# Optimization experiments

Hardware: AMD Instinct MI355X
Metric: run time of the kernel (lower is better)

The kernel has to match this reference:

```python
import jax, jax.numpy as jnp
import numpy as np

EPS_LN = 1e-5


def fwht(x):
    """Fast Walsh-Hadamard transform over the last axis (power-of-two length).
    Vectorized butterfly: log2(n) stages, each a reshape + add/sub."""
    orig_shape = x.shape
    n = orig_shape[-1]
    y = x.reshape(-1, n)
    h = 1
    while h < n:
        y = y.reshape(-1, n // (2 * h), 2, h)
        a = y[:, :, 0, :]
        b = y[:, :, 1, :]
        y = jnp.stack([a + b, a - b], axis=2).reshape(-1, n)
        h <<= 1
    return y.reshape(orig_shape)


def setup_inputs() -> dict:
    key = jax.random.key(0)
    kx, kw, kg = jax.random.split(key, 3)
    B, S, D_IN, D_OUT = 4, 4096, 2048, 2048
    x = jax.random.normal(kx, (B, S, D_IN), dtype=jnp.float32)
    # kaiming_uniform_(a=sqrt(5)) -> bound = 1/sqrt(in_features)
    bound = 1.0 / np.sqrt(D_IN)
    W = jax.random.uniform(kw, (D_OUT, D_IN), dtype=jnp.float32,
                           minval=-bound, maxval=bound)
    gamma = jnp.ones((D_IN,), dtype=jnp.float32)
    beta = jnp.zeros((D_IN,), dtype=jnp.float32)
    return {"x": x, "W": W, "gamma": gamma, "beta": beta}


def reference(x, W, gamma, beta):
    bits = 4
    max_val = (1 << (bits - 1)) - 1  # 7
    # LayerNorm over last dim
    mu = jnp.mean(x, axis=-1, keepdims=True)
    var = jnp.mean(jnp.square(x - mu), axis=-1, keepdims=True)
    x_ln = (x - mu) * jax.lax.rsqrt(var + EPS_LN) * gamma + beta
    # Activation fake-quant to `bits` bits (per-row absmax scale)
    x_scale = jnp.clip(jnp.max(jnp.abs(x_ln), axis=-1, keepdims=True), 1e-6, None)
    x_int = jnp.clip(jnp.round(x_ln * max_val / x_scale), -max_val, max_val)
    x_q = x_int * x_scale / max_val
    # Hadamard transform of quantized activations
    x_h = fwht(x_q)
    # Ternary weight quantization with global mean-abs scale
    w_scale = jnp.clip(jnp.mean(jnp.abs(W)), 1e-6, None)
    w_q = (jnp.where(W > 0.5 * w_scale, 1.0, 0.0)
           + jnp.where(W < -0.5 * w_scale, -1.0, 0.0)) * w_scale
    # Linear (no bias), then second Hadamard transform
    out = jnp.einsum('bsd,od->bso', x_h, w_q)
    return fwht(out)
```

## Files before the change

### kernel.cpp

```cpp
#include <hip/hip_runtime.h>

typedef unsigned short u16;
typedef __attribute__((ext_vector_type(8))) __bf16 bf16x8;
typedef __attribute__((ext_vector_type(16))) float floatx16;

#define DDIM 2048
#define MROWS 16384
#define BK 64

__device__ __forceinline__ u16 f2bf(float f) {
    unsigned int u = __builtin_bit_cast(unsigned int, f);
    u = (u + 0x7fffu + ((u >> 16) & 1u)) >> 16;
    return (u16)u;
}

__device__ __forceinline__ float wave_sum(float v) {
#pragma unroll
    for (int o = 32; o > 0; o >>= 1) v += __shfl_down(v, o, 64);
    return v;
}
__device__ __forceinline__ float wave_max(float v) {
#pragma unroll
    for (int o = 32; o > 0; o >>= 1) v = fmaxf(v, __shfl_down(v, o, 64));
    return v;
}

__global__ __launch_bounds__(256) void absmean_part(const float4* __restrict__ W4,
                                                    float* __restrict__ partial) {
    float s = 0.f;
    for (int i = blockIdx.x * 256 + threadIdx.x; i < (DDIM * DDIM / 4); i += 1024 * 256) {
        float4 v = W4[i];
        s += fabsf(v.x) + fabsf(v.y) + fabsf(v.z) + fabsf(v.w);
    }
    s = wave_sum(s);
    __shared__ float red[4];
    if ((threadIdx.x & 63) == 0) red[threadIdx.x >> 6] = s;
    __syncthreads();
    if (threadIdx.x == 0) partial[blockIdx.x] = red[0] + red[1] + red[2] + red[3];
}

template <bool QUANT>
__global__ __launch_bounds__(256) void transpose_k(const float* __restrict__ in,
                                                   float* __restrict__ out,
                                                   const float* __restrict__ partial) {
    __shared__ float tile[64][65];
    const int t = threadIdx.x;
    float wsc = 0.f, half_t = 0.f;
    if (QUANT) {
        __shared__ float wred[4];
        float s = partial[t] + partial[t + 256] + partial[t + 512] + partial[t + 768];
        s = wave_sum(s);
        if ((t & 63) == 0) wred[t >> 6] = s;
        __syncthreads();
        float m = (wred[0] + wred[1] + wred[2] + wred[3]) * (1.0f / (float)(DDIM * DDIM));
        wsc = fmaxf(m, 1e-6f);
        half_t = 0.5f * wsc;
        __syncthreads();
    }
    const int tx = t & 63;
    const int ty = t >> 6;
    const int r0 = blockIdx.y * 64;
    const int c0 = blockIdx.x * 64;
#pragma unroll
    for (int i = 0; i < 16; ++i) {
        int r = ty + i * 4;
        float w = in[(size_t)(r0 + r) * DDIM + c0 + tx];
        if (QUANT) w = (w > half_t ? wsc : 0.f) + (w < -half_t ? -wsc : 0.f);
        tile[r][tx] = w;
    }
    __syncthreads();
#pragma unroll
    for (int i = 0; i < 16; ++i) {
        int r = ty + i * 4;
        out[(size_t)(c0 + r) * DDIM + r0 + tx] = tile[tx][r];
    }
}

template <bool BF16OUT>
__global__ __launch_bounds__(256) void fwht_rows(const float* __restrict__ in,
                                                 void* __restrict__ out) {
    __shared__ float s0[DDIM];
    __shared__ float s1[DDIM];
    const int row = blockIdx.x;
    const int t = threadIdx.x;
    const int lane = t & 63;
    const float4* rp = (const float4*)(in + (size_t)row * DDIM);
    float4 a = rp[t], b = rp[t + 256];
    float v[8] = {a.x, a.y, a.z, a.w, b.x, b.y, b.z, b.w};

#pragma unroll
    for (int h = 1; h <= 4; h <<= 1)
#pragma unroll
        for (int j = 0; j < 8; ++j)
            if (!(j & h)) { float x = v[j], y = v[j | h]; v[j] = x + y; v[j | h] = x - y; }

#pragma unroll
    for (int m = 1; m <= 32; m <<= 1)
#pragma unroll
        for (int j = 0; j < 8; ++j) {
            float p = __shfl_xor(v[j], m, 64);
            v[j] = (lane & m) ? (p - v[j]) : (p + v[j]);
        }

    ((float4*)s0)[2 * t] = make_float4(v[0], v[1], v[2], v[3]);
    ((float4*)s0)[2 * t + 1] = make_float4(v[4], v[5], v[6], v[7]);
    __syncthreads();
    {
        int p1 = t ^ 64;
        float4 pa = ((const float4*)s0)[2 * p1], pb = ((const float4*)s0)[2 * p1 + 1];
        float pv[8] = {pa.x, pa.y, pa.z, pa.w, pb.x, pb.y, pb.z, pb.w};
#pragma unroll
        for (int j = 0; j < 8; ++j) v[j] = (t & 64) ? (pv[j] - v[j]) : (pv[j] + v[j]);
    }
    ((float4*)s1)[2 * t] = make_float4(v[0], v[1], v[2], v[3]);
    ((float4*)s1)[2 * t + 1] = make_float4(v[4], v[5], v[6], v[7]);
    __syncthreads();
    {
        int p2 = t ^ 128;
        float4 pa = ((const float4*)s1)[2 * p2], pb = ((const float4*)s1)[2 * p2 + 1];
        float pv[8] = {pa.x, pa.y, pa.z, pa.w, pb.x, pb.y, pb.z, pb.w};
#pragma unroll
        for (int j = 0; j < 8; ++j) v[j] = (t & 128) ? (pv[j] - v[j]) : (pv[j] + v[j]);
    }

    if (BF16OUT) {
        u16* op = (u16*)out + (size_t)row * DDIM;
        uint2 o0, o1;
        o0.x = (unsigned)f2bf(v[0]) | ((unsigned)f2bf(v[1]) << 16);
        o0.y = (unsigned)f2bf(v[2]) | ((unsigned)f2bf(v[3]) << 16);
        o1.x = (unsigned)f2bf(v[4]) | ((unsigned)f2bf(v[5]) << 16);
        o1.y = (unsigned)f2bf(v[6]) | ((unsigned)f2bf(v[7]) << 16);
        ((uint2*)op)[t] = o0;
        ((uint2*)op)[t + 256] = o1;
    } else {
        float* op = (float*)out + (size_t)row * DDIM;
        ((float4*)op)[t] = make_float4(v[0], v[1], v[2], v[3]);
        ((float4*)op)[t + 256] = make_float4(v[4], v[5], v[6], v[7]);
    }
}

__global__ __launch_bounds__(256) void ln_quant(const float* __restrict__ X,
                                                const float* __restrict__ G,
                                                const float* __restrict__ Bt,
                                                u16* __restrict__ XQ) {
    const int row = blockIdx.x;
    const int t = threadIdx.x;
    const float4* rp = (const float4*)(X + (size_t)row * DDIM);
    float4 v0 = rp[t], v1 = rp[t + 256];
    float v[8] = {v0.x, v0.y, v0.z, v0.w, v1.x, v1.y, v1.z, v1.w};

    __shared__ float redA[4], redB[4], redC[4];
    const int wv = t >> 6, ln = t & 63;

    float s = 0.f, s2 = 0.f;
#pragma unroll
    for (int j = 0; j < 8; ++j) { s += v[j]; s2 += v[j] * v[j]; }
#pragma unroll
    for (int o = 32; o > 0; o >>= 1) {
        s += __shfl_down(s, o, 64);
        s2 += __shfl_down(s2, o, 64);
    }
    if (ln == 0) { redA[wv] = s; redB[wv] = s2; }
    __syncthreads();
    const float mu = (redA[0] + redA[1] + redA[2] + redA[3]) * (1.f / (float)DDIM);
    const float ex2 = (redB[0] + redB[1] + redB[2] + redB[3]) * (1.f / (float)DDIM);
    const float var = ex2 - mu * mu;
    const float rstd = rsqrtf(var + 1e-5f);

    const float4* gp = (const float4*)G;
    const float4* bp = (const float4*)Bt;
    float4 g0 = gp[t], g1 = gp[t + 256];
    float4 b0 = bp[t], b1 = bp[t + 256];
    float gg[8] = {g0.x, g0.y, g0.z, g0.w, g1.x, g1.y, g1.z, g1.w};
    float bb[8] = {b0.x, b0.y, b0.z, b0.w, b1.x, b1.y, b1.z, b1.w};

    float y[8];
    float am = 0.f;
#pragma unroll
    for (int j = 0; j < 8; ++j) {
        y[j] = (v[j] - mu) * rstd * gg[j] + bb[j];
        am = fmaxf(am, fabsf(y[j]));
    }
    float w = wave_max(am);
    if (ln == 0) redC[wv] = w;
    __syncthreads();
    const float scale = fmaxf(fmaxf(fmaxf(redC[0], redC[1]), fmaxf(redC[2], redC[3])), 1e-6f);

    const float r7 = 7.f / scale, s7 = scale / 7.f;
    unsigned int q[4];
#pragma unroll
    for (int j = 0; j < 8; j += 2) {
        float qa = fminf(fmaxf(rintf(y[j] * r7), -7.f), 7.f);
        float qb = fminf(fmaxf(rintf(y[j + 1] * r7), -7.f), 7.f);
        q[j >> 1] = (unsigned)f2bf(qa * s7) | ((unsigned)f2bf(qb * s7) << 16);
    }
    uint2 o0, o1;
    o0.x = q[0]; o0.y = q[1]; o1.x = q[2]; o1.y = q[3];
    uint2* orow = (uint2*)(XQ + (size_t)row * DDIM);
    orow[t] = o0;
    orow[t + 256] = o1;
}

__device__ __forceinline__ void gl_lds16(const u16* g, u16* l) {
    __builtin_amdgcn_global_load_lds((const __attribute__((address_space(1))) void*)g,
                                     (__attribute__((address_space(3))) void*)l,
                                     16, 0, 0);
}

__global__ __launch_bounds__(256) void gemm_bt(const u16* __restrict__ A,
                                               const u16* __restrict__ B,
                                               float* __restrict__ C) {
    __shared__ __align__(16) u16 As[128 * BK];
    __shared__ __align__(16) u16 Bs[128 * BK];
    const int bm = blockIdx.y, bn = blockIdx.x;
    const int t = threadIdx.x;
    const int wave = t >> 6, lane = t & 63;
    const int m_off = (wave >> 1) << 6;
    const int n_off = (wave & 1) << 6;
    const int l31 = lane & 31, lh = lane >> 5;

    floatx16 acc[2][2];
#pragma unroll
    for (int mi = 0; mi < 2; ++mi)
#pragma unroll
        for (int ni = 0; ni < 2; ++ni)
#pragma unroll
            for (int e = 0; e < 16; ++e) acc[mi][ni][e] = 0.f;

    const int srow = t >> 3;
    const int sc = ((t & 7) ^ (srow & 7)) << 3;
    const u16* Ag = A + (size_t)(bm * 128 + srow) * DDIM + sc;
    const u16* Bg = B + (size_t)(bn * 128 + srow) * DDIM + sc;
    u16* Asl = As + t * 8;
    u16* Bsl = Bs + t * 8;

    for (int kt = 0; kt < DDIM / BK; ++kt) {
        const size_t ko = (size_t)kt * BK;
#pragma unroll
        for (int i = 0; i < 4; ++i) {
            gl_lds16(Ag + (size_t)(i * 32) * DDIM + ko, Asl + i * 2048);
            gl_lds16(Bg + (size_t)(i * 32) * DDIM + ko, Bsl + i * 2048);
        }
        __syncthreads();

#pragma unroll
        for (int ks = 0; ks < 4; ++ks) {
            const int swz = ((ks * 2 + lh) ^ (l31 & 7)) << 3;
            bf16x8 af[2], bfr[2];
#pragma unroll
            for (int mi = 0; mi < 2; ++mi)
                af[mi] = *(const bf16x8*)(As + (m_off + mi * 32 + l31) * BK + swz);
#pragma unroll
            for (int ni = 0; ni < 2; ++ni)
                bfr[ni] = *(const bf16x8*)(Bs + (n_off + ni * 32 + l31) * BK + swz);
#pragma unroll
            for (int mi = 0; mi < 2; ++mi)
#pragma unroll
                for (int ni = 0; ni < 2; ++ni)
                    acc[mi][ni] = __builtin_amdgcn_mfma_f32_32x32x16_bf16(af[mi], bfr[ni],
                                                                          acc[mi][ni], 0, 0, 0);
        }
        __syncthreads();
    }

    float* Cb = C + (size_t)(bm * 128 + m_off) * DDIM + bn * 128 + n_off;
#pragma unroll
    for (int mi = 0; mi < 2; ++mi)
#pragma unroll
        for (int ni = 0; ni < 2; ++ni)
#pragma unroll
            for (int r = 0; r < 16; ++r) {
                const int rl = (r & 3) + 8 * (r >> 2) + 4 * lh;
                Cb[(size_t)(mi * 32 + rl) * DDIM + ni * 32 + l31] = acc[mi][ni][r];
            }
}

extern "C" void kernel_launch(void* const* d_in, const int* in_sizes, int n_in,
                              void* d_out, int out_size, void* d_ws, size_t ws_size,
                              hipStream_t stream) {
    const float* X  = (const float*)d_in[0];
    const float* W  = (const float*)d_in[1];
    const float* G  = (const float*)d_in[2];
    const float* Bt = (const float*)d_in[3];
    float* out = (float*)d_out;

    char* ws = (char*)d_ws;
    u16*   xq   = (u16*)ws;
    float* bufA = (float*)(ws + (size_t)67108864);
    float* bufB = (float*)(ws + (size_t)67108864 + 16777216);
    float* partial = bufB;
    u16*   w3      = (u16*)bufB;

    absmean_part<<<1024, 256, 0, stream>>>((const float4*)W, partial);
    transpose_k<true><<<dim3(32, 32), 256, 0, stream>>>(W, bufA, partial);
    fwht_rows<false><<<2048, 256, 0, stream>>>(bufA, (void*)bufB);
    transpose_k<false><<<dim3(32, 32), 256, 0, stream>>>(bufB, bufA, nullptr);
    fwht_rows<true><<<2048, 256, 0, stream>>>(bufA, (void*)w3);
    ln_quant<<<MROWS, 256, 0, stream>>>(X, G, Bt, xq);
    gemm_bt<<<dim3(16, 128), 256, 0, stream>>>(xq, w3, out);
}
```

Baseline: 412.8 us.

## Replace GEMM with 256x256 double-buffered, ping-pong scheduled MFMA kernel

```diff
diff --git a/kernel.cpp b/kernel.cpp
--- a/kernel.cpp
+++ b/kernel.cpp
@@ -2,11 +2,10 @@
 
 typedef unsigned short u16;
 typedef __attribute__((ext_vector_type(8))) __bf16 bf16x8;
-typedef __attribute__((ext_vector_type(16))) float floatx16;
+typedef __attribute__((ext_vector_type(4))) float floatx4;
 
 #define DDIM 2048
 #define MROWS 16384
-#define BK 64
 
 __device__ __forceinline__ u16 f2bf(float f) {
     unsigned int u = __builtin_bit_cast(unsigned int, f);
@@ -201,78 +200,144 @@
     orow[t + 256] = o1;
 }
 
+#define GBK 64
+#define GNT (DDIM / GBK)
+#define TILEU (256 * GBK)
+
 __device__ __forceinline__ void gl_lds16(const u16* g, u16* l) {
     __builtin_amdgcn_global_load_lds((const __attribute__((address_space(1))) void*)g,
                                      (__attribute__((address_space(3))) void*)l,
                                      16, 0, 0);
 }
 
-__global__ __launch_bounds__(256) void gemm_bt(const u16* __restrict__ A,
-                                               const u16* __restrict__ B,
-                                               float* __restrict__ C) {
-    __shared__ __align__(16) u16 As[128 * BK];
-    __shared__ __align__(16) u16 Bs[128 * BK];
-    const int bm = blockIdx.y, bn = blockIdx.x;
+__device__ __forceinline__ void pbar() {
+    __builtin_amdgcn_sched_barrier(0);
+    asm volatile("" ::: "memory");
+    __builtin_amdgcn_s_barrier();
+    asm volatile("" ::: "memory");
+    __builtin_amdgcn_sched_barrier(0);
+}
+
+__global__ __launch_bounds__(512, 2) void gemm256(const u16* __restrict__ A,
+                                                  const u16* __restrict__ B,
+                                                  float* __restrict__ C) {
+    extern __shared__ __align__(16) u16 lds[];
     const int t = threadIdx.x;
-    const int wave = t >> 6, lane = t & 63;
-    const int m_off = (wave >> 1) << 6;
-    const int n_off = (wave & 1) << 6;
-    const int l31 = lane & 31, lh = lane >> 5;
-
-    floatx16 acc[2][2];
-#pragma unroll
-    for (int mi = 0; mi < 2; ++mi)
-#pragma unroll
-        for (int ni = 0; ni < 2; ++ni)
-#pragma unroll
-            for (int e = 0; e < 16; ++e) acc[mi][ni][e] = 0.f;
+    const int lane = t & 63;
+    const int wid = t >> 6;
+    const int wm = wid >> 2;
+    const int wn = wid & 3;
+
+    const int d = blockIdx.x;
+    const int bm = (d & 7) | ((d >> 6) << 3);
+    const int bn = (d >> 3) & 7;
+
+    const int l15 = lane & 15;
+    const int kq = lane >> 4;
+    const int x7 = lane & 7;
+    const int c0 = (kq ^ x7) << 3;
+    const int c1 = ((kq | 4) ^ x7) << 3;
+    const int arow = (wm << 7) + l15;
+    const int brow = (wn << 6) + l15;
 
     const int srow = t >> 3;
-    const int sc = ((t & 7) ^ (srow & 7)) << 3;
-    const u16* Ag = A + (size_t)(bm * 128 + srow) * DDIM + sc;
-    const u16* Bg = B + (size_t)(bn * 128 + srow) * DDIM + sc;
-    u16* Asl = As + t * 8;
-    u16* Bsl = Bs + t * 8;
-
-    for (int kt = 0; kt < DDIM / BK; ++kt) {
-        const size_t ko = (size_t)kt * BK;
-#pragma unroll
-        for (int i = 0; i < 4; ++i) {
-            gl_lds16(Ag + (size_t)(i * 32) * DDIM + ko, Asl + i * 2048);
-            gl_lds16(Bg + (size_t)(i * 32) * DDIM + ko, Bsl + i * 2048);
+    const int gch = ((t & 7) ^ (srow & 7)) << 3;
+    const u16* Ag = A + (size_t)(bm * 256 + srow) * DDIM + gch;
+    const u16* Bg = B + (size_t)(bn * 256 + srow) * DDIM + gch;
+
+    floatx4 acc[8][4];
+#pragma unroll
+    for (int i = 0; i < 8; ++i)
+#pragma unroll
+        for (int j = 0; j < 4; ++j)
+#pragma unroll
+            for (int e = 0; e < 4; ++e) acc[i][j][e] = 0.f;
+
+    bf16x8 a[4][2], b0v[2][2], b1v[2][2];
+
+#define STAGE(gb, ldsoff, ko)                                                  \
+    _Pragma("unroll") for (int q = 0; q < 4; ++q)                              \
+        gl_lds16((gb) + (size_t)(q * 64) * DDIM + (ko),                        \
+                 lds + (ldsoff) + q * 4096 + t * 8);
+
+#define LDA(mh)                                                                \
+    _Pragma("unroll") for (int fm = 0; fm < 4; ++fm) {                         \
+        const u16* p = Ab + (arow + (mh) * 64 + fm * 16) * GBK;                \
+        a[fm][0] = *(const bf16x8*)(p + c0);                                   \
+        a[fm][1] = *(const bf16x8*)(p + c1);                                   \
+    }
+
+#define LDB(dst, nh)                                                           \
+    _Pragma("unroll") for (int fn = 0; fn < 2; ++fn) {                         \
+        const u16* p = Bb + (brow + (nh) * 32 + fn * 16) * GBK;                \
+        dst[fn][0] = *(const bf16x8*)(p + c0);                                 \
+        dst[fn][1] = *(const bf16x8*)(p + c1);                                 \
+    }
+
+#define MMA(mh, bsrc, nh)                                                      \
+    __builtin_amdgcn_s_setprio(1);                                             \
+    _Pragma("unroll") for (int fm = 0; fm < 4; ++fm)                           \
+        _Pragma("unroll") for (int fn = 0; fn < 2; ++fn)                       \
+            _Pragma("unroll") for (int ks = 0; ks < 2; ++ks)                   \
+                acc[(mh) * 4 + fm][(nh) * 2 + fn] =                            \
+                    __builtin_amdgcn_mfma_f32_16x16x32_bf16(                   \
+                        a[fm][ks], bsrc[fn][ks],                               \
+                        acc[(mh) * 4 + fm][(nh) * 2 + fn], 0, 0, 0);           \
+    __builtin_amdgcn_s_setprio(0);
+
+    STAGE(Ag, 0, 0);
+    STAGE(Bg, TILEU, 0);
+    STAGE(Ag, 2 * TILEU, GBK);
+    STAGE(Bg, 3 * TILEU, GBK);
+    __builtin_amdgcn_sched_barrier(0);
+    asm volatile("s_waitcnt vmcnt(8)");
+    pbar();
+
+    for (int kt = 0; kt < GNT; ++kt) {
+        const int boff = (kt & 1) * (2 * TILEU);
+        const u16* Ab = lds + boff;
+        const u16* Bb = lds + boff + TILEU;
+
+        LDA(0);
+        LDB(b0v, 0);
+        pbar();
+        MMA(0, b0v, 0);
+        pbar();
+        LDB(b1v, 1);
+        pbar();
+        MMA(0, b1v, 1);
+        pbar();
+        LDA(1);
+        if (kt + 2 < GNT) { STAGE(Bg, boff + TILEU, (kt + 2) * GBK); }
+        pbar();
+        MMA(1, b0v, 0);
+        pbar();
+        if (kt + 2 < GNT) { STAGE(Ag, boff, (kt + 2) * GBK); }
+        pbar();
+        MMA(1, b1v, 1);
+        __builtin_amdgcn_sched_barrier(0);
+        if (kt < GNT - 2) {
+            asm volatile("s_waitcnt vmcnt(8)");
+        } else {
+            asm volatile("s_waitcnt vmcnt(0)");
         }
-        __syncthreads();
-
-#pragma unroll
-        for (int ks = 0; ks < 4; ++ks) {
-            const int swz = ((ks * 2 + lh) ^ (l31 & 7)) << 3;
-            bf16x8 af[2], bfr[2];
-#pragma unroll
-            for (int mi = 0; mi < 2; ++mi)
-                af[mi] = *(const bf16x8*)(As + (m_off + mi * 32 + l31) * BK + swz);
-#pragma unroll
-            for (int ni = 0; ni < 2; ++ni)
-                bfr[ni] = *(const bf16x8*)(Bs + (n_off + ni * 32 + l31) * BK + swz);
-#pragma unroll
-            for (int mi = 0; mi < 2; ++mi)
-#pragma unroll
-                for (int ni = 0; ni < 2; ++ni)
-                    acc[mi][ni] = __builtin_amdgcn_mfma_f32_32x32x16_bf16(af[mi], bfr[ni],
-                                                                          acc[mi][ni], 0, 0, 0);
-        }
-        __syncthreads();
-    }
-
-    float* Cb = C + (size_t)(bm * 128 + m_off) * DDIM + bn * 128 + n_off;
-#pragma unroll
-    for (int mi = 0; mi < 2; ++mi)
-#pragma unroll
-        for (int ni = 0; ni < 2; ++ni)
-#pragma unroll
-            for (int r = 0; r < 16; ++r) {
-                const int rl = (r & 3) + 8 * (r >> 2) + 4 * lh;
-                Cb[(size_t)(mi * 32 + rl) * DDIM + ni * 32 + l31] = acc[mi][ni][r];
-            }
+        pbar();
+    }
+
+#undef STAGE
+#undef LDA
+#undef LDB
+#undef MMA
+
+    float* Cb = C + (size_t)(bm * 256 + (wm << 7) + (lane >> 4) * 4) * DDIM
+                  + bn * 256 + (wn << 6) + l15;
+#pragma unroll
+    for (int fm = 0; fm < 8; ++fm)
+#pragma unroll
+        for (int fn = 0; fn < 4; ++fn)
+#pragma unroll
+            for (int r = 0; r < 4; ++r)
+                Cb[(size_t)(fm * 16 + r) * DDIM + fn * 16] = acc[fm][fn][r];
 }
 
 extern "C" void kernel_launch(void* const* d_in, const int* in_sizes, int n_in,
@@ -297,5 +362,7 @@
     transpose_k<false><<<dim3(32, 32), 256, 0, stream>>>(bufB, bufA, nullptr);
     fwht_rows<true><<<2048, 256, 0, stream>>>(bufA, (void*)w3);
     ln_quant<<<MROWS, 256, 0, stream>>>(X, G, Bt, xq);
-    gemm_bt<<<dim3(16, 128), 256, 0, stream>>>(xq, w3, out);
-}
+    hipFuncSetAttribute(reinterpret_cast<const void*>(gemm256),
+                        hipFuncAttributeMaxDynamicSharedMemorySize, 131072);
+    gemm256<<<dim3(512), 512, 131072, stream>>>(xq, w3, out);
+}
```

Measured after the change: 398.2 us. 3.5% less time.
